# Kernel optimization log

Hardware: AMD Instinct MI355X
Metric: run time of the kernel (lower is better)

Reference implementation:

```python
import jax, jax.numpy as jnp
import numpy as np

K = 1024
D = 256
BETA = 0.25


def setup_inputs() -> dict:
    key = jax.random.key(0)
    k1, k2 = jax.random.split(key)
    inputs = jax.random.normal(k1, (16, D, 4096), dtype=jnp.float32)  # (B, D, T)
    # embedding.weight.data.uniform_(-1/K, 1/K)
    weight = jax.random.uniform(k2, (K, D), dtype=jnp.float32, minval=-1.0 / K, maxval=1.0 / K)
    return {"inputs": inputs, "weight": weight}


def reference(inputs, weight):
    B, Dd, T = inputs.shape
    x = jnp.transpose(inputs, (0, 2, 1))          # (B, T, D)
    flat = x.reshape(-1, Dd)                      # (N, D), N = B*T
    in_sqr = jnp.sum(flat * flat, axis=1, keepdims=True)     # (N, 1)
    embed_sqr = jnp.sum(weight * weight, axis=1)             # (K,)
    dis = in_sqr + embed_sqr - 2.0 * (flat @ weight.T)       # (N, K)
    ind = jnp.argmin(dis, axis=1)                            # (N,)
    quant = weight[ind].reshape(B, T, Dd)                    # gather == one-hot @ weight
    vq = jnp.mean((jax.lax.stop_gradient(quant) - x) ** 2)
    commit = jnp.mean((quant - jax.lax.stop_gradient(x)) ** 2)
    vq_loss = BETA * vq + commit
    quant_st = x + jax.lax.stop_gradient(quant - x)          # straight-through
    N = flat.shape[0]
    counts = jnp.zeros((K,), dtype=jnp.float32).at[ind].add(1.0)
    avg_probs = counts / N
    perp = jnp.exp(-jnp.sum(avg_probs * jnp.log(avg_probs + 1e-10)))
    return jnp.transpose(quant_st, (0, 2, 1)), vq_loss, perp
```

## Files before the change

kernel.cpp:

```cpp
#include <hip/hip_runtime.h>
#include <hip/hip_bf16.h>


#define DD   256
#define KK   1024
#define TT   4096
#define BBB  16
#define NROW (BBB*TT)

typedef _Float16 half8 __attribute__((ext_vector_type(8)));
typedef float f32x4 __attribute__((ext_vector_type(4)));

__device__ __forceinline__ unsigned umaxu(unsigned a, unsigned b) { return a > b ? a : b; }
__device__ __forceinline__ unsigned uminu(unsigned a, unsigned b) { return a < b ? a : b; }

__global__ void prep(const float* __restrict__ w, _Float16* __restrict__ w16,
                     unsigned* __restrict__ counts, double* __restrict__ lsum,
                     float* __restrict__ wsq) {
    int gid = blockIdx.x * 256 + threadIdx.x;
    int k = gid >> 5;
    int c = gid & 31;
    int chunk = k >> 4, n = k & 15;
    int ks = c >> 2, q = c & 3;
    const float* src = w + (k << 8) + (c << 3);
    union { uint4 u; _Float16 h[8]; } pk;
#pragma unroll
    for (int j = 0; j < 8; ++j) pk.h[j] = (_Float16)(src[j] * 1024.0f);
    size_t dst = ((((size_t)chunk * 8 + ks) * 4 + q) * 16 + n) * 8;
    *(uint4*)(w16 + dst) = pk.u;
    if (c == 0) {
        const float4* wr4 = (const float4*)(w + (k << 8));
        float s = 0.f;
#pragma unroll 8
        for (int ii = 0; ii < 64; ++ii) {
            float4 v = wr4[ii];
            s += v.x * v.x + v.y * v.y + v.z * v.z + v.w * v.w;
        }
        wsq[k] = 512.0f * s;
    }
    if (gid < KK) counts[gid] = 0u;
    if (gid == KK) *lsum = 0.0;
}

#define XLS 257

#define XLOAD(toff) do {                                                       \
    int _dr = tid >> 3;                                                        \
    int _t4 = (tid & 7) << 2;                                                  \
    const float* _xb = x + ((size_t)b << 20) + t0 + (toff) + _t4;              \
    _Pragma("unroll")                                                          \
    for (int _pass = 0; _pass < 8; ++_pass) {                                  \
        int _d = (_pass << 5) + _dr;                                           \
        float4 _v = *(const float4*)(_xb + ((size_t)_d << 12));                \
        xt[(_t4 + 0) * XLS + _d] = _v.x;                                       \
        xt[(_t4 + 1) * XLS + _d] = _v.y;                                       \
        xt[(_t4 + 2) * XLS + _d] = _v.z;                                       \
        xt[(_t4 + 3) * XLS + _d] = _v.w;                                       \
    }                                                                          \
} while (0)

#define LOADB(PFX, chn) do {                                                   \
    const uint4* _p = wsrc + ((chn) << 9) + lane;                              \
    PFX##0 = *(const half8*)(_p);                                              \
    PFX##1 = *(const half8*)(_p + 64);                                         \
    PFX##2 = *(const half8*)(_p + 128);                                        \
    PFX##3 = *(const half8*)(_p + 192);                                        \
    PFX##4 = *(const half8*)(_p + 256);                                        \
    PFX##5 = *(const half8*)(_p + 320);                                        \
    PFX##6 = *(const half8*)(_p + 384);                                        \
    PFX##7 = *(const half8*)(_p + 448);                                        \
} while (0)

#define MFMA16(A, B, C) __builtin_amdgcn_mfma_f32_16x16x32_f16((A), (B), (C), 0, 0, 0)

#define COMPUTE(ch, PFX) do {                                                  \
    f32x4 a0 = {0.f, 0.f, 0.f, 0.f};                                           \
    f32x4 a1 = {0.f, 0.f, 0.f, 0.f};                                           \
    a0 = MFMA16(afrag[0][0], PFX##0, a0); a1 = MFMA16(afrag[1][0], PFX##0, a1);\
    a0 = MFMA16(afrag[0][1], PFX##1, a0); a1 = MFMA16(afrag[1][1], PFX##1, a1);\
    a0 = MFMA16(afrag[0][2], PFX##2, a0); a1 = MFMA16(afrag[1][2], PFX##2, a1);\
    a0 = MFMA16(afrag[0][3], PFX##3, a0); a1 = MFMA16(afrag[1][3], PFX##3, a1);\
    a0 = MFMA16(afrag[0][4], PFX##4, a0); a1 = MFMA16(afrag[1][4], PFX##4, a1);\
    a0 = MFMA16(afrag[0][5], PFX##5, a0); a1 = MFMA16(afrag[1][5], PFX##5, a1);\
    a0 = MFMA16(afrag[0][6], PFX##6, a0); a1 = MFMA16(afrag[1][6], PFX##6, a1);\
    a0 = MFMA16(afrag[0][7], PFX##7, a0); a1 = MFMA16(afrag[1][7], PFX##7, a1);\
    unsigned kg = (unsigned)(((ch) << 4) + n);                                 \
    float csub = wsql[kg];                                                     \
    _Pragma("unroll")                                                          \
    for (int i = 0; i < 4; ++i) {                                              \
        float v; unsigned p, o;                                                \
        v = fmaxf(a0[i] - csub, 0.0f);                                         \
        p = (__float_as_uint(v) & 0xFFFFFC00u) | kg;                           \
        o = b1[i];                                                             \
        b2[i] = umaxu(b2[i], uminu(p, o));                                     \
        b1[i] = umaxu(o, p);                                                   \
        v = fmaxf(a1[i] - csub, 0.0f);                                         \
        p = (__float_as_uint(v) & 0xFFFFFC00u) | kg;                           \
        o = b1[4 + i];                                                         \
        b2[4 + i] = umaxu(b2[4 + i], uminu(p, o));                             \
        b1[4 + i] = umaxu(o, p);                                               \
    }                                                                          \
} while (0)

__global__ __launch_bounds__(256, 2) void fused(const float* __restrict__ x,
                                                const float* __restrict__ w,
                                                const _Float16* __restrict__ w16,
                                                const float* __restrict__ wsq,
                                                float* __restrict__ out,
                                                unsigned* __restrict__ counts,
                                                double* __restrict__ lsum) {
    __shared__ __align__(16) float xt[32 * XLS];
    __shared__ __align__(16) float wsql[KK];
    __shared__ __align__(16) uint4 cndl[128];
    __shared__ double disl[32][4];
    __shared__ int winner[32];
    __shared__ double ldis[32];

    int tid = threadIdx.x, bid = blockIdx.x;
    int b = bid >> 5;
    int t0 = (bid & 31) << 7;
    int lane = tid & 63, wv = tid >> 6;
    int n = lane & 15, q = lane >> 4;

    ((float4*)wsql)[tid] = ((const float4*)wsq)[tid];

    half8 afrag[2][8];
#pragma unroll
    for (int p = 0; p < 4; ++p) {
        XLOAD(p << 5);
        __syncthreads();
        if (wv == p) {
#pragma unroll
            for (int mt = 0; mt < 2; ++mt) {
                int rl = (mt << 4) + n;
#pragma unroll
                for (int ks = 0; ks < 8; ++ks) {
                    const float* sp = &xt[rl * XLS + (ks << 5) + (q << 3)];
                    half8 f;
#pragma unroll
                    for (int j = 0; j < 8; ++j) f[j] = (_Float16)sp[j];
                    afrag[mt][ks] = f;
                }
            }
        }
        __syncthreads();
    }

    unsigned b1[8], b2[8];
#pragma unroll
    for (int i = 0; i < 8; ++i) { b1[i] = 0u; b2[i] = 0u; }

    const uint4* wsrc = (const uint4*)w16;
    half8 bA0, bA1, bA2, bA3, bA4, bA5, bA6, bA7;
    half8 bB0, bB1, bB2, bB3, bB4, bB5, bB6, bB7;

    LOADB(bA, 0);
    for (int ch = 0; ch < 64; ch += 2) {
        LOADB(bB, ch + 1);
        COMPUTE(ch, bA);
        if (ch + 2 < 64) LOADB(bA, ch + 2);
        COMPUTE(ch + 1, bB);
    }

#pragma unroll
    for (int s = 0; s < 8; ++s) {
        unsigned v0 = b1[s], v1 = b2[s], v2 = 0u, v3 = 0u;
#pragma unroll
        for (int m = 1; m <= 8; m <<= 1) {
            unsigned e0 = __shfl_xor(v0, m);
            unsigned e1 = __shfl_xor(v1, m);
            unsigned e2 = __shfl_xor(v2, m);
            unsigned e3 = __shfl_xor(v3, m);
#pragma unroll
            for (int u = 0; u < 4; ++u) {
                unsigned e = (u == 0) ? e0 : (u == 1) ? e1 : (u == 2) ? e2 : e3;
                unsigned t;
                t = umaxu(e, v0); e = uminu(e, v0); v0 = t;
                t = umaxu(e, v1); e = uminu(e, v1); v1 = t;
                t = umaxu(e, v2); e = uminu(e, v2); v2 = t;
                v3 = umaxu(e, v3);
            }
        }
        if (n == 0) {
            int row_local = (wv << 5) + ((s >> 2) << 4) + (q << 2) + (s & 3);
            cndl[row_local] = make_uint4(v0, v1, v2, v3);
        }
    }
    __syncthreads();

    int c = lane >> 4, dl = lane & 15;
    int rr2 = lane >> 3, c8 = lane & 7;
    for (int qt = 0; qt < 4; ++qt) {
        XLOAD(qt << 5);
        __syncthreads();

#pragma unroll
        for (int rr = 0; rr < 8; ++rr) {
            int r = (wv << 3) + rr;
            unsigned ci = ((const unsigned*)cndl)[(((qt << 5) + r) << 2) + c] & 1023u;
            const float* wr = w + (ci << 8);
            double s = 0.0;
#pragma unroll
            for (int dd = 0; dd < 4; ++dd) {
                int d4 = (dd << 6) + (dl << 2);
                float4 xv = *(const float4*)(&xt[r * XLS + d4]);
                float4 wv4 = *(const float4*)(wr + d4);
                double e;
                e = (double)xv.x - (double)wv4.x; s = fma(e, e, s);
                e = (double)xv.y - (double)wv4.y; s = fma(e, e, s);
                e = (double)xv.z - (double)wv4.z; s = fma(e, e, s);
                e = (double)xv.w - (double)wv4.w; s = fma(e, e, s);
            }
#pragma unroll
            for (int m = 1; m <= 8; m <<= 1) s += __shfl_xor(s, m);
            if (dl == 0) disl[r][c] = s;
        }
        __syncthreads();

        if (tid < 32) {
            uint4 cc = cndl[(qt << 5) + tid];
            unsigned i0 = cc.x & 1023u, i1 = cc.y & 1023u, i2 = cc.z & 1023u, i3 = cc.w & 1023u;
            double dm = disl[tid][0]; unsigned ci = i0;
            double dk;
            dk = disl[tid][1]; if (dk < dm || (dk == dm && i1 < ci)) { dm = dk; ci = i1; }
            dk = disl[tid][2]; if (dk < dm || (dk == dm && i2 < ci)) { dm = dk; ci = i2; }
            dk = disl[tid][3]; if (dk < dm || (dk == dm && i3 < ci)) { dm = dk; ci = i3; }
            winner[tid] = (int)ci;
            ldis[tid] = dm;
            atomicAdd(&counts[ci], 1u);
        }
        __syncthreads();

        {
            int rowr = (wv << 3) + rr2;
            int win = winner[rowr];
            const float* wrow = w + (win << 8);
#pragma unroll
            for (int cc2 = 0; cc2 < 4; ++cc2) {
                int col = (cc2 << 6) + (c8 << 3);
                float4 g0 = *(const float4*)(wrow + col);
                float4 g1 = *(const float4*)(wrow + col + 4);
                *(float4*)(&xt[rowr * XLS + col]) = g0;
                *(float4*)(&xt[rowr * XLS + col + 4]) = g1;
            }
        }
        __syncthreads();

        {
            int dr = tid >> 3;
            int t4 = (tid & 7) << 2;
            float* ob = out + ((size_t)b << 20) + t0 + (qt << 5) + t4;
#pragma unroll
            for (int pass = 0; pass < 8; ++pass) {
                int d = (pass << 5) + dr;
                float4 o;
                o.x = xt[(t4 + 0) * XLS + d];
                o.y = xt[(t4 + 1) * XLS + d];
                o.z = xt[(t4 + 2) * XLS + d];
                o.w = xt[(t4 + 3) * XLS + d];
                *(float4*)(ob + ((size_t)d << 12)) = o;
            }
        }

        __syncthreads();
        if (tid < 16) ldis[tid] += ldis[tid + 16];
        __syncthreads();
        if (tid < 8) ldis[tid] += ldis[tid + 8];
        __syncthreads();
        if (tid < 4) ldis[tid] += ldis[tid + 4];
        __syncthreads();
        if (tid < 2) ldis[tid] += ldis[tid + 2];
        __syncthreads();
        if (tid == 0) atomicAdd(lsum, ldis[0] + ldis[1]);
        __syncthreads();
    }
}

__global__ void finalize(const unsigned* __restrict__ counts,
                         const double* __restrict__ lsum,
                         float* __restrict__ out2) {
    __shared__ double part[256];
    int tid = threadIdx.x;
    double s = 0.0;
    for (int i = tid; i < KK; i += 256) {
        double p = (double)counts[i] / (double)NROW;
        s += p * log(p + 1e-10);
    }
    part[tid] = s;
    __syncthreads();
    for (int st = 128; st > 0; st >>= 1) {
        if (tid < st) part[tid] += part[tid + st];
        __syncthreads();
    }
    if (tid == 0) {
        out2[0] = (float)(1.25 * (*lsum) / ((double)NROW * (double)DD));
        out2[1] = (float)exp(-part[0]);
    }
}

extern "C" void kernel_launch(void* const* d_in, const int* in_sizes, int n_in,
                              void* d_out, int out_size, void* d_ws, size_t ws_size,
                              hipStream_t stream) {
    const float* x = (const float*)d_in[0];
    const float* w = (const float*)d_in[1];
    float* out = (float*)d_out;
    char* ws = (char*)d_ws;
    _Float16* w16    = (_Float16*)ws;
    unsigned* counts = (unsigned*)(ws + 524288);
    float*    wsq    = (float*)(ws + 528384);
    double*   lsum   = (double*)(ws + 532480);

    prep<<<128, 256, 0, stream>>>(w, w16, counts, lsum, wsq);
    fused<<<512, 256, 0, stream>>>(x, w, w16, wsq, out, counts, lsum);
    finalize<<<1, 256, 0, stream>>>(counts, lsum, out + (size_t)NROW * DD);
}
```

Measured before the change: 182.1 us.

## Split codebook search across two wave halves with 512-thread blocks

Doubles the block to 512 threads so that two groups of four waves each scan half of the codebook chunks. Each group keeps its own top-2 candidates, and the exact fp64 rescoring then takes 8 candidates per row. The ldis shared-memory tree reduction with its many barriers is replaced by a wave shuffle reduction, and __syncthreads is swapped for a lighter lgkmcnt wait plus s_barrier. The aim is more parallelism per block and fewer sync points, at the cost of higher register pressure under launch_bounds(512,4) and twice the candidate rescoring work.

```diff
diff --git a/kernel.cpp b/kernel.cpp
--- a/kernel.cpp
+++ b/kernel.cpp
@@ -13,6 +13,12 @@
 
 __device__ __forceinline__ unsigned umaxu(unsigned a, unsigned b) { return a > b ? a : b; }
 __device__ __forceinline__ unsigned uminu(unsigned a, unsigned b) { return a < b ? a : b; }
+
+__device__ __forceinline__ void barrier_lgkm() {
+    asm volatile("s_waitcnt lgkmcnt(0)" ::: "memory");
+    __builtin_amdgcn_s_barrier();
+    __builtin_amdgcn_sched_barrier(0);
+}
 
 __global__ void prep(const float* __restrict__ w, _Float16* __restrict__ w16,
                      unsigned* __restrict__ counts, double* __restrict__ lsum,
@@ -45,12 +51,12 @@
 #define XLS 257
 
 #define XLOAD(toff) do {                                                       \
-    int _dr = tid >> 3;                                                        \
-    int _t4 = (tid & 7) << 2;                                                  \
+    int _dr = tid >> 3;                                             \
+    int _t4 = (tid & 7) << 2;                                       \
     const float* _xb = x + ((size_t)b << 20) + t0 + (toff) + _t4;              \
     _Pragma("unroll")                                                          \
-    for (int _pass = 0; _pass < 8; ++_pass) {                                  \
-        int _d = (_pass << 5) + _dr;                                           \
+    for (int _pass = 0; _pass < 4; ++_pass) {                                  \
+        int _d = (_pass << 6) + _dr;                               \
         float4 _v = *(const float4*)(_xb + ((size_t)_d << 12));                \
         xt[(_t4 + 0) * XLS + _d] = _v.x;                                       \
         xt[(_t4 + 1) * XLS + _d] = _v.y;                                       \
@@ -102,7 +108,7 @@
     }                                                                          \
 } while (0)
 
-__global__ __launch_bounds__(256, 2) void fused(const float* __restrict__ x,
+__global__ __launch_bounds__(512, 4) void fused(const float* __restrict__ x,
                                                 const float* __restrict__ w,
                                                 const _Float16* __restrict__ w16,
                                                 const float* __restrict__ wsq,
@@ -111,25 +117,26 @@
                                                 double* __restrict__ lsum) {
     __shared__ __align__(16) float xt[32 * XLS];
     __shared__ __align__(16) float wsql[KK];
-    __shared__ __align__(16) uint4 cndl[128];
-    __shared__ double disl[32][4];
+    __shared__ __align__(16) uint4 cndl[128][2];
+    __shared__ double disl[32][8];
     __shared__ int winner[32];
-    __shared__ double ldis[32];
 
     int tid = threadIdx.x, bid = blockIdx.x;
     int b = bid >> 5;
     int t0 = (bid & 31) << 7;
     int lane = tid & 63, wv = tid >> 6;
+    int h = wv >> 2;
+    int wq = wv & 3;
     int n = lane & 15, q = lane >> 4;
 
-    ((float4*)wsql)[tid] = ((const float4*)wsq)[tid];
+    ((float2*)wsql)[tid] = ((const float2*)wsq)[tid];
 
     half8 afrag[2][8];
 #pragma unroll
     for (int p = 0; p < 4; ++p) {
         XLOAD(p << 5);
         __syncthreads();
-        if (wv == p) {
+        if (wq == p) {
 #pragma unroll
             for (int mt = 0; mt < 2; ++mt) {
                 int rl = (mt << 4) + n;
@@ -151,15 +158,16 @@
     for (int i = 0; i < 8; ++i) { b1[i] = 0u; b2[i] = 0u; }
 
     const uint4* wsrc = (const uint4*)w16;
+    int h32 = h << 5;
     half8 bA0, bA1, bA2, bA3, bA4, bA5, bA6, bA7;
     half8 bB0, bB1, bB2, bB3, bB4, bB5, bB6, bB7;
 
-    LOADB(bA, 0);
-    for (int ch = 0; ch < 64; ch += 2) {
-        LOADB(bB, ch + 1);
-        COMPUTE(ch, bA);
-        if (ch + 2 < 64) LOADB(bA, ch + 2);
-        COMPUTE(ch + 1, bB);
+    LOADB(bA, h32);
+    for (int ch = 0; ch < 32; ch += 2) {
+        LOADB(bB, h32 + ch + 1);
+        COMPUTE(h32 + ch, bA);
+        if (ch + 2 < 32) LOADB(bA, h32 + ch + 2);
+        COMPUTE(h32 + ch + 1, bB);
     }
 
 #pragma unroll
@@ -182,27 +190,27 @@
             }
         }
         if (n == 0) {
-            int row_local = (wv << 5) + ((s >> 2) << 4) + (q << 2) + (s & 3);
-            cndl[row_local] = make_uint4(v0, v1, v2, v3);
+            int row_local = (wq << 5) + ((s >> 2) << 4) + (q << 2) + (s & 3);
+            cndl[row_local][h] = make_uint4(v0, v1, v2, v3);
         }
     }
     __syncthreads();
 
-    int c = lane >> 4, dl = lane & 15;
+    int c = lane >> 3, dl = lane & 7;
     int rr2 = lane >> 3, c8 = lane & 7;
     for (int qt = 0; qt < 4; ++qt) {
         XLOAD(qt << 5);
-        __syncthreads();
-
-#pragma unroll
-        for (int rr = 0; rr < 8; ++rr) {
-            int r = (wv << 3) + rr;
-            unsigned ci = ((const unsigned*)cndl)[(((qt << 5) + r) << 2) + c] & 1023u;
+        barrier_lgkm();
+
+#pragma unroll
+        for (int rr = 0; rr < 4; ++rr) {
+            int r = (wv << 2) + rr;
+            unsigned ci = ((const unsigned*)cndl)[(((qt << 5) + r) << 3) + c] & 1023u;
             const float* wr = w + (ci << 8);
             double s = 0.0;
 #pragma unroll
-            for (int dd = 0; dd < 4; ++dd) {
-                int d4 = (dd << 6) + (dl << 2);
+            for (int dd = 0; dd < 8; ++dd) {
+                int d4 = (dd << 5) + (dl << 2);
                 float4 xv = *(const float4*)(&xt[r * XLS + d4]);
                 float4 wv4 = *(const float4*)(wr + d4);
                 double e;
@@ -211,27 +219,38 @@
                 e = (double)xv.z - (double)wv4.z; s = fma(e, e, s);
                 e = (double)xv.w - (double)wv4.w; s = fma(e, e, s);
             }
-#pragma unroll
-            for (int m = 1; m <= 8; m <<= 1) s += __shfl_xor(s, m);
+            s += __shfl_xor(s, 1);
+            s += __shfl_xor(s, 2);
+            s += __shfl_xor(s, 4);
             if (dl == 0) disl[r][c] = s;
         }
-        __syncthreads();
-
-        if (tid < 32) {
-            uint4 cc = cndl[(qt << 5) + tid];
-            unsigned i0 = cc.x & 1023u, i1 = cc.y & 1023u, i2 = cc.z & 1023u, i3 = cc.w & 1023u;
-            double dm = disl[tid][0]; unsigned ci = i0;
-            double dk;
-            dk = disl[tid][1]; if (dk < dm || (dk == dm && i1 < ci)) { dm = dk; ci = i1; }
-            dk = disl[tid][2]; if (dk < dm || (dk == dm && i2 < ci)) { dm = dk; ci = i2; }
-            dk = disl[tid][3]; if (dk < dm || (dk == dm && i3 < ci)) { dm = dk; ci = i3; }
-            winner[tid] = (int)ci;
-            ldis[tid] = dm;
-            atomicAdd(&counts[ci], 1u);
-        }
-        __syncthreads();
+        barrier_lgkm();
 
         {
+            double dm = 0.0;
+            if (tid < 32) {
+                const unsigned* cp = ((const unsigned*)cndl) + (((qt << 5) + tid) << 3);
+                double dmv = disl[tid][0];
+                unsigned ci = cp[0] & 1023u;
+                for (int j = 1; j < 8; ++j) {
+                    double dk = disl[tid][j];
+                    unsigned cj = cp[j] & 1023u;
+                    if (dk < dmv || (dk == dmv && cj < ci)) { dmv = dk; ci = cj; }
+                }
+                winner[tid] = (int)ci;
+                dm = dmv;
+                atomicAdd(&counts[ci], 1u);
+            }
+            if (wv == 0) {
+                dm += __shfl_xor(dm, 16); dm += __shfl_xor(dm, 8);
+                dm += __shfl_xor(dm, 4);  dm += __shfl_xor(dm, 2);
+                dm += __shfl_xor(dm, 1);  dm += __shfl_xor(dm, 32);
+                if (lane == 0) atomicAdd(lsum, dm);
+            }
+        }
+        barrier_lgkm();
+
+        if (wv < 4) {
             int rowr = (wv << 3) + rr2;
             int win = winner[rowr];
             const float* wrow = w + (win << 8);
@@ -244,15 +263,15 @@
                 *(float4*)(&xt[rowr * XLS + col + 4]) = g1;
             }
         }
-        __syncthreads();
+        barrier_lgkm();
 
         {
             int dr = tid >> 3;
             int t4 = (tid & 7) << 2;
             float* ob = out + ((size_t)b << 20) + t0 + (qt << 5) + t4;
 #pragma unroll
-            for (int pass = 0; pass < 8; ++pass) {
-                int d = (pass << 5) + dr;
+            for (int pass = 0; pass < 4; ++pass) {
+                int d = (pass << 6) + dr;
                 float4 o;
                 o.x = xt[(t4 + 0) * XLS + d];
                 o.y = xt[(t4 + 1) * XLS + d];
@@ -261,18 +280,7 @@
                 *(float4*)(ob + ((size_t)d << 12)) = o;
             }
         }
-
-        __syncthreads();
-        if (tid < 16) ldis[tid] += ldis[tid + 16];
-        __syncthreads();
-        if (tid < 8) ldis[tid] += ldis[tid + 8];
-        __syncthreads();
-        if (tid < 4) ldis[tid] += ldis[tid + 4];
-        __syncthreads();
-        if (tid < 2) ldis[tid] += ldis[tid + 2];
-        __syncthreads();
-        if (tid == 0) atomicAdd(lsum, ldis[0] + ldis[1]);
-        __syncthreads();
+        barrier_lgkm();
     }
 }
 
@@ -311,6 +319,6 @@
     double*   lsum   = (double*)(ws + 532480);
 
     prep<<<128, 256, 0, stream>>>(w, w16, counts, lsum, wsq);
-    fused<<<512, 256, 0, stream>>>(x, w, w16, wsq, out, counts, lsum);
+    fused<<<512, 512, 0, stream>>>(x, w, w16, wsq, out, counts, lsum);
     finalize<<<1, 256, 0, stream>>>(counts, lsum, out + (size_t)NROW * DD);
 }
```

After: 379.2 us. 2.08x slower.
